# Kernel tuning notes

Measured on AMD Instinct MI355X. Metric: run time of the kernel, lower is better.

## Reference

```python
import jax, jax.numpy as jnp
import numpy as np

N_USERS = 150000
N_ENTITIES = 250000
CH = 64
N_REL = 17
N_FACTORS = 4
N_EDGES = 1_000_000
NNZ = 1_000_000
N_HOPS = 2


def setup_inputs() -> dict:
    key = jax.random.key(0)
    ks = jax.random.split(key, 10)
    user_emb = jax.random.normal(ks[0], (N_USERS, CH), jnp.float32) * 0.1
    entity_emb = jax.random.normal(ks[1], (N_ENTITIES, CH), jnp.float32) * 0.1
    latent_emb = jax.random.normal(ks[2], (N_FACTORS, CH), jnp.float32) * 0.1
    weight = jax.random.normal(ks[3], (N_REL - 1, CH), jnp.float32) * 0.1
    disen_weight_att = jax.random.normal(ks[4], (N_FACTORS, N_REL - 1), jnp.float32) * 0.1
    edge_index = jax.random.randint(ks[5], (2, N_EDGES), 0, N_ENTITIES)
    edge_type = jax.random.randint(ks[6], (N_EDGES,), 1, N_REL)  # in [1, N_REL-1]
    inter_row = jax.random.randint(ks[7], (NNZ,), 0, N_USERS)
    inter_col = jax.random.randint(ks[8], (NNZ,), 0, N_ENTITIES)
    inter_val = jax.random.uniform(ks[9], (NNZ,), jnp.float32)
    return {
        "user_emb": user_emb, "entity_emb": entity_emb, "latent_emb": latent_emb,
        "weight": weight, "disen_weight_att": disen_weight_att, "inter_val": inter_val,
        "edge_index": edge_index, "edge_type": edge_type,
        "inter_row": inter_row, "inter_col": inter_col,
    }


def _l2norm(x):
    # F.normalize(x, dim=1) with eps=1e-12
    n = jnp.linalg.norm(x, axis=1, keepdims=True)
    return x / jnp.maximum(n, 1e-12)


def reference(user_emb, entity_emb, latent_emb, weight, disen_weight_att,
              inter_val, edge_index, edge_type, inter_row, inter_col):
    n_entities = entity_emb.shape[0]
    n_users = user_emb.shape[0]
    head, tail = edge_index[0], edge_index[1]

    # _cul_cor with ind='cosine': sum_{i<j} cos(w_i, w_j)^2 over rows of disen_weight_att
    wn = disen_weight_att / jnp.linalg.norm(disen_weight_att, axis=1, keepdims=True)
    gram = (wn @ wn.T) ** 2  # [F, F]
    cor = jnp.sum(jnp.triu(gram, k=1))

    # constants across hops
    counts = jax.ops.segment_sum(jnp.ones(head.shape[0], jnp.float32), head,
                                 num_segments=n_entities)
    denom = jnp.maximum(counts, 1.0)[:, None]  # scatter_mean denominator (0 -> keep 0)
    disen_weight = jax.nn.softmax(disen_weight_att, axis=-1) @ weight  # [F, C]

    e, u = entity_emb, user_emb
    ent_res, usr_res = entity_emb, user_emb
    for _ in range(N_HOPS):
        # KG aggregate: per-edge gather, relation modulation, scatter_mean into heads
        neigh = e[tail] * weight[edge_type - 1]              # [E, C]
        entity_agg = jax.ops.segment_sum(neigh, head, num_segments=n_entities) / denom

        # user -> latent factor attention
        score = jax.nn.softmax(u @ latent_emb.T, axis=1)[:, :, None]  # [U, F, 1]

        # user aggregate: sparse interact_mat @ entity_emb
        user_agg = jax.ops.segment_sum(inter_val[:, None] * e[inter_col], inter_row,
                                       num_segments=n_users)  # [U, C]
        mix = jnp.sum(disen_weight[None, :, :] * score, axis=1)  # [U, C]
        user_agg = user_agg * mix + user_agg

        e = _l2norm(entity_agg)
        u = _l2norm(user_agg)
        ent_res = ent_res + e
        usr_res = usr_res + u
    return ent_res, usr_res, cor
```

## Files before the change

### kernel.cpp

```cpp
#include <hip/hip_runtime.h>
#include <hip/hip_bf16.h>

#define N_USERS    150000
#define N_ENTITIES 250000
#define CHN        64
#define N_RELM1    16
#define N_FACTORS  4
#define N_EDGES    1000000
#define NNZ_       1000000
#define NRECS      (N_EDGES + NNZ_)

#define BROWS      1024
#define RCAP       8192
#define RCAP_OUT   8192
#define EBUCKETS   245
#define USR0       (EBUCKETS * BROWS)
#define ROWS_EFF   (USR0 + N_USERS)
#define NB         392
#define TILE_A     4096
#define TA_THREADS 512
#define ITEMS_A    8

typedef float vf4 __attribute__((ext_vector_type(4)));

__device__ __forceinline__ unsigned short f2bf(float f) {
    unsigned u = __float_as_uint(f);
    return (unsigned short)((u + 0x7fffu + ((u >> 16) & 1u)) >> 16);
}

__global__ __launch_bounds__(512) void prep_small_kernel(const float* __restrict__ weight,
                                  const float* __restrict__ att,
                                  float* __restrict__ disenw,
                                  float* __restrict__ cor_out,
                                  int* __restrict__ bcur)
{
    int tid = threadIdx.x;
    if (tid < NB) bcur[tid] = tid * RCAP;

    if (tid < 256) {
        int f  = tid >> 6;
        int ch = tid & 63;
        float m = -1e30f;
        for (int r = 0; r < N_RELM1; ++r) m = fmaxf(m, att[f * N_RELM1 + r]);
        float ex[N_RELM1];
        float s = 0.f;
        for (int r = 0; r < N_RELM1; ++r) { ex[r] = expf(att[f * N_RELM1 + r] - m); s += ex[r]; }
        float inv = 1.f / s;
        float acc = 0.f;
        for (int r = 0; r < N_RELM1; ++r) acc += (ex[r] * inv) * weight[r * CHN + ch];
        disenw[f * CHN + ch] = acc;
    }

    if (tid == 0) {
        float wn[N_FACTORS][N_RELM1];
        for (int i = 0; i < N_FACTORS; ++i) {
            float ss = 0.f;
            for (int r = 0; r < N_RELM1; ++r) { float v = att[i * N_RELM1 + r]; ss += v * v; }
            float innv = 1.f / sqrtf(ss);
            for (int r = 0; r < N_RELM1; ++r) wn[i][r] = att[i * N_RELM1 + r] * innv;
        }
        float cor = 0.f;
        for (int i = 0; i < N_FACTORS; ++i)
            for (int j = i + 1; j < N_FACTORS; ++j) {
                float d = 0.f;
                for (int r = 0; r < N_RELM1; ++r) d += wn[i][r] * wn[j][r];
                cor += d * d;
            }
        cor_out[0] = cor;
    }
}

__global__ __launch_bounds__(256) void conv_bf16_kernel(const float4* __restrict__ src,
                                                        ushort4* __restrict__ dst, int n4)
{
    int i = blockIdx.x * 256 + threadIdx.x;
    if (i >= n4) return;
    float4 v = src[i];
    dst[i] = make_ushort4(f2bf(v.x), f2bf(v.y), f2bf(v.z), f2bf(v.w));
}

__global__ __launch_bounds__(TA_THREADS) void bin_pass_kernel(
    const int* __restrict__ head, const int* __restrict__ tail,
    const int* __restrict__ etype, const int* __restrict__ irow,
    const int* __restrict__ icol, const float* __restrict__ val,
    int* __restrict__ bcur, unsigned long long* __restrict__ binned)
{
    __shared__ int cntS[NB], startS[NB], gbase[NB];
    __shared__ unsigned long long buf[TILE_A];
    __shared__ unsigned short bk[TILE_A];

    int tid = threadIdx.x;
    if (tid < NB) cntS[tid] = 0;
    __syncthreads();

    int base = blockIdx.x * TILE_A;
    unsigned long long p[ITEMS_A];
    int bkt[ITEMS_A], rnk[ITEMS_A];
    #pragma unroll
    for (int j = 0; j < ITEMS_A; ++j) {
        int i = base + j * TA_THREADS + tid;
        bkt[j] = -1;
        if (i < NRECS) {
            int row; unsigned long long pay;
            if (i < N_EDGES) {
                row = head[i];
                pay = ((unsigned long long)(unsigned)(etype[i] - 1) << 18) | (unsigned)tail[i];
            } else {
                int jj = i - N_EDGES;
                row = USR0 + irow[jj];
                pay = ((unsigned long long)__float_as_uint(val[jj]) << 18) | (unsigned)icol[jj];
            }
            p[j] = pay | ((unsigned long long)(unsigned)(row & (BROWS - 1)) << 50);
            bkt[j] = row >> 10;
            rnk[j] = atomicAdd(&cntS[bkt[j]], 1);
        }
    }
    __syncthreads();
    if (tid == 0) {
        int s = 0;
        for (int b = 0; b < NB; ++b) { startS[b] = s; s += cntS[b]; }
    }
    __syncthreads();
    if (tid < NB && cntS[tid] > 0) gbase[tid] = atomicAdd(&bcur[tid], cntS[tid]);
    __syncthreads();

    #pragma unroll
    for (int j = 0; j < ITEMS_A; ++j) {
        if (bkt[j] >= 0) {
            int s = startS[bkt[j]] + rnk[j];
            buf[s] = p[j];
            bk[s] = (unsigned short)bkt[j];
        }
    }
    __syncthreads();

    int total = startS[NB - 1] + cntS[NB - 1];
    for (int s = tid; s < total; s += TA_THREADS) {
        int b = bk[s];
        int dst = gbase[b] + (s - startS[b]);
        if (dst < (b + 1) * RCAP) binned[dst] = buf[s];
    }
}

__global__ __launch_bounds__(512) void bucket_scatter_kernel(
    const unsigned long long* __restrict__ binned,
    const int* __restrict__ bcur,
    unsigned int* __restrict__ recsE,
    unsigned long long* __restrict__ recsU,
    unsigned int* __restrict__ cntoffs)
{
    __shared__ int rowcnt[BROWS];
    __shared__ int sA[512], sB[512];

    int tid = threadIdx.x;
    int b = blockIdx.x;
    rowcnt[2 * tid] = 0;
    rowcnt[2 * tid + 1] = 0;
    __syncthreads();

    int s0 = b * RCAP;
    int s1 = bcur[b];
    if (s1 > s0 + RCAP) s1 = s0 + RCAP;

    for (int i = s0 + tid; i < s1; i += 512) {
        int rowlo = (int)(binned[i] >> 50) & (BROWS - 1);
        atomicAdd(&rowcnt[rowlo], 1);
    }
    __syncthreads();

    int c0 = rowcnt[2 * tid];
    int c1 = rowcnt[2 * tid + 1];
    int pc0 = (c0 + 1) & ~1;
    int pc1 = (c1 + 1) & ~1;
    sA[tid] = pc0 + pc1;
    __syncthreads();
    int* src = sA; int* dst = sB;
    #pragma unroll
    for (int off = 1; off < 512; off <<= 1) {
        dst[tid] = src[tid] + ((tid >= off) ? src[tid - off] : 0);
        __syncthreads();
        int* tm = src; src = dst; dst = tm;
    }
    int excl = src[tid] - (pc0 + pc1);

    int gbaseOut = (b < EBUCKETS ? b : b - EBUCKETS) * RCAP_OUT;
    int grow = b * BROWS;
    cntoffs[grow + 2 * tid]     = ((unsigned)c0 << 22) | (unsigned)(gbaseOut + excl);
    cntoffs[grow + 2 * tid + 1] = ((unsigned)c1 << 22) | (unsigned)(gbaseOut + excl + pc0);
    __syncthreads();
    rowcnt[2 * tid] = excl;
    rowcnt[2 * tid + 1] = excl + pc0;
    __syncthreads();

    if (b < EBUCKETS) {
        for (int i = s0 + tid; i < s1; i += 512) {
            unsigned long long p = binned[i];
            int rowlo = (int)(p >> 50) & (BROWS - 1);
            int local = atomicAdd(&rowcnt[rowlo], 1);
            recsE[gbaseOut + local] = (unsigned)(p & ((1ull << 50) - 1));
        }
    } else {
        for (int i = s0 + tid; i < s1; i += 512) {
            unsigned long long p = binned[i];
            int rowlo = (int)(p >> 50) & (BROWS - 1);
            int local = atomicAdd(&rowcnt[rowlo], 1);
            recsU[gbaseOut + local] = p & ((1ull << 50) - 1);
        }
    }
}

__device__ __forceinline__ void fma8w(uint4 g, const float* __restrict__ w, float* acc) {
    acc[0] += __uint_as_float(g.x << 16)          * w[0];
    acc[1] += __uint_as_float(g.x & 0xffff0000u)  * w[1];
    acc[2] += __uint_as_float(g.y << 16)          * w[2];
    acc[3] += __uint_as_float(g.y & 0xffff0000u)  * w[3];
    acc[4] += __uint_as_float(g.z << 16)          * w[4];
    acc[5] += __uint_as_float(g.z & 0xffff0000u)  * w[5];
    acc[6] += __uint_as_float(g.w << 16)          * w[6];
    acc[7] += __uint_as_float(g.w & 0xffff0000u)  * w[7];
}
__device__ __forceinline__ void fma8v(uint4 g, float v, float* acc) {
    acc[0] += __uint_as_float(g.x << 16)          * v;
    acc[1] += __uint_as_float(g.x & 0xffff0000u)  * v;
    acc[2] += __uint_as_float(g.y << 16)          * v;
    acc[3] += __uint_as_float(g.y & 0xffff0000u)  * v;
    acc[4] += __uint_as_float(g.z << 16)          * v;
    acc[5] += __uint_as_float(g.z & 0xffff0000u)  * v;
    acc[6] += __uint_as_float(g.w << 16)          * v;
    acc[7] += __uint_as_float(g.w & 0xffff0000u)  * v;
}
__device__ __forceinline__ void bf8_unpack(uint4 g, float* o) {
    o[0] = __uint_as_float(g.x << 16); o[1] = __uint_as_float(g.x & 0xffff0000u);
    o[2] = __uint_as_float(g.y << 16); o[3] = __uint_as_float(g.y & 0xffff0000u);
    o[4] = __uint_as_float(g.z << 16); o[5] = __uint_as_float(g.z & 0xffff0000u);
    o[6] = __uint_as_float(g.w << 16); o[7] = __uint_as_float(g.w & 0xffff0000u);
}

template<int PASS>
__global__ __launch_bounds__(256) void hop_kernel(
    const unsigned short* __restrict__ ebf,
    const unsigned int* __restrict__ recsE,
    const unsigned long long* __restrict__ recsU,
    const unsigned int* __restrict__ cntoffs,
    const float* __restrict__ weight,
    const float* __restrict__ latent,
    const float* __restrict__ disenw,
    const float* __restrict__ u_emb,
    const float* __restrict__ e_emb,
    const unsigned short* __restrict__ ubfA,
    unsigned short* __restrict__ ebf_new,
    unsigned short* __restrict__ ubf_new,
    float* __restrict__ out_ent,
    float* __restrict__ out_usr)
{
    __shared__ float wl[N_RELM1 * CHN];
    for (int k = threadIdx.x; k < N_RELM1 * CHN; k += 256) wl[k] = weight[k];
    __syncthreads();

    unsigned idx = blockIdx.x * 256u + threadIdx.x;
    unsigned row = idx >> 3;
    int sub = idx & 7;
    int chb = sub * 8;

    float acc[8] = {0.f,0.f,0.f,0.f,0.f,0.f,0.f,0.f};

    if (row < N_ENTITIES) {
        unsigned co = cntoffs[row];
        int n = co >> 22;
        int start = co & 0x3FFFFF;
        int k = 0;
        for (; k + 4 <= n; k += 4) {
            uint2 ra = *(const uint2*)&recsE[start + k];
            uint2 rb = *(const uint2*)&recsE[start + k + 2];
            uint4 g0 = *(const uint4*)(ebf + (size_t)(ra.x & 0x3FFFF) * CHN + chb);
            uint4 g1 = *(const uint4*)(ebf + (size_t)(ra.y & 0x3FFFF) * CHN + chb);
            uint4 g2 = *(const uint4*)(ebf + (size_t)(rb.x & 0x3FFFF) * CHN + chb);
            uint4 g3 = *(const uint4*)(ebf + (size_t)(rb.y & 0x3FFFF) * CHN + chb);
            fma8w(g0, &wl[(ra.x >> 18) * CHN + chb], acc);
            fma8w(g1, &wl[(ra.y >> 18) * CHN + chb], acc);
            fma8w(g2, &wl[(rb.x >> 18) * CHN + chb], acc);
            fma8w(g3, &wl[(rb.y >> 18) * CHN + chb], acc);
        }
        for (; k < n; ++k) {
            unsigned r0 = recsE[start + k];
            uint4 g0 = *(const uint4*)(ebf + (size_t)(r0 & 0x3FFFF) * CHN + chb);
            fma8w(g0, &wl[(r0 >> 18) * CHN + chb], acc);
        }
        float inv_d = (n > 0) ? (1.f / (float)n) : 1.f;
        float ss = 0.f;
        #pragma unroll
        for (int i = 0; i < 8; ++i) { acc[i] *= inv_d; ss += acc[i] * acc[i]; }
        ss += __shfl_xor(ss, 1, 64);
        ss += __shfl_xor(ss, 2, 64);
        ss += __shfl_xor(ss, 4, 64);
        float innv = 1.f / fmaxf(sqrtf(ss), 1e-12f);
        float y[8];
        #pragma unroll
        for (int i = 0; i < 8; ++i) y[i] = acc[i] * innv;
        if (PASS == 1) {
            uint4 pk;
            pk.x = (unsigned)f2bf(y[0]) | ((unsigned)f2bf(y[1]) << 16);
            pk.y = (unsigned)f2bf(y[2]) | ((unsigned)f2bf(y[3]) << 16);
            pk.z = (unsigned)f2bf(y[4]) | ((unsigned)f2bf(y[5]) << 16);
            pk.w = (unsigned)f2bf(y[6]) | ((unsigned)f2bf(y[7]) << 16);
            *(uint4*)(ebf_new + (size_t)row * CHN + chb) = pk;
        } else {
            float y1[8];
            bf8_unpack(*(const uint4*)(ebf + (size_t)row * CHN + chb), y1);
            const vf4* bp = (const vf4*)&e_emb[(size_t)row * CHN + chb];
            vf4 b0 = __builtin_nontemporal_load(bp);
            vf4 b1 = __builtin_nontemporal_load(bp + 1);
            vf4* op = (vf4*)&out_ent[(size_t)row * CHN + chb];
            vf4 o0 = {b0.x + y1[0] + y[0], b0.y + y1[1] + y[1], b0.z + y1[2] + y[2], b0.w + y1[3] + y[3]};
            vf4 o1 = {b1.x + y1[4] + y[4], b1.y + y1[5] + y[5], b1.z + y1[6] + y[6], b1.w + y1[7] + y[7]};
            __builtin_nontemporal_store(o0, op);
            __builtin_nontemporal_store(o1, op + 1);
        }
    } else if (row >= USR0 && row < ROWS_EFF) {
        unsigned ur = row - USR0;
        unsigned co = cntoffs[row];
        int n = co >> 22;
        int start = co & 0x3FFFFF;

        float uo[8];
        if (PASS == 1) {
            const float4* up = (const float4*)&u_emb[(size_t)ur * CHN + chb];
            float4 a0 = up[0], a1 = up[1];
            uo[0]=a0.x; uo[1]=a0.y; uo[2]=a0.z; uo[3]=a0.w;
            uo[4]=a1.x; uo[5]=a1.y; uo[6]=a1.z; uo[7]=a1.w;
        } else {
            bf8_unpack(*(const uint4*)(ubfA + (size_t)ur * CHN + chb), uo);
        }

        float dotv[N_FACTORS];
        #pragma unroll
        for (int f = 0; f < N_FACTORS; ++f) {
            const float4* lp = (const float4*)&latent[f * CHN + chb];
            float4 l0 = lp[0], l1 = lp[1];
            float p = uo[0] * l0.x + uo[1] * l0.y + uo[2] * l0.z + uo[3] * l0.w
                    + uo[4] * l1.x + uo[5] * l1.y + uo[6] * l1.z + uo[7] * l1.w;
            p += __shfl_xor(p, 1, 64);
            p += __shfl_xor(p, 2, 64);
            p += __shfl_xor(p, 4, 64);
            dotv[f] = p;
        }
        float m = fmaxf(fmaxf(dotv[0], dotv[1]), fmaxf(dotv[2], dotv[3]));
        float es = 0.f;
        #pragma unroll
        for (int f = 0; f < N_FACTORS; ++f) { dotv[f] = expf(dotv[f] - m); es += dotv[f]; }
        float sinv = 1.f / es;
        float mix[8] = {0.f,0.f,0.f,0.f,0.f,0.f,0.f,0.f};
        #pragma unroll
        for (int f = 0; f < N_FACTORS; ++f) {
            float sc = dotv[f] * sinv;
            const float4* dp = (const float4*)&disenw[f * CHN + chb];
            float4 d0 = dp[0], d1 = dp[1];
            mix[0] += sc * d0.x; mix[1] += sc * d0.y; mix[2] += sc * d0.z; mix[3] += sc * d0.w;
            mix[4] += sc * d1.x; mix[5] += sc * d1.y; mix[6] += sc * d1.z; mix[7] += sc * d1.w;
        }

        int k = 0;
        for (; k + 4 <= n; k += 4) {
            ulonglong2 qa = *(const ulonglong2*)&recsU[start + k];
            ulonglong2 qb = *(const ulonglong2*)&recsU[start + k + 2];
            uint4 g0 = *(const uint4*)(ebf + (size_t)(qa.x & 0x3FFFFu) * CHN + chb);
            uint4 g1 = *(const uint4*)(ebf + (size_t)(qa.y & 0x3FFFFu) * CHN + chb);
            uint4 g2 = *(const uint4*)(ebf + (size_t)(qb.x & 0x3FFFFu) * CHN + chb);
            uint4 g3 = *(const uint4*)(ebf + (size_t)(qb.y & 0x3FFFFu) * CHN + chb);
            fma8v(g0, __uint_as_float((unsigned)(qa.x >> 18)), acc);
            fma8v(g1, __uint_as_float((unsigned)(qa.y >> 18)), acc);
            fma8v(g2, __uint_as_float((unsigned)(qb.x >> 18)), acc);
            fma8v(g3, __uint_as_float((unsigned)(qb.y >> 18)), acc);
        }
        for (; k < n; ++k) {
            unsigned long long q0 = recsU[start + k];
            uint4 g0 = *(const uint4*)(ebf + (size_t)(q0 & 0x3FFFFu) * CHN + chb);
            fma8v(g0, __uint_as_float((unsigned)(q0 >> 18)), acc);
        }
        float ss = 0.f;
        #pragma unroll
        for (int i = 0; i < 8; ++i) { acc[i] *= (1.f + mix[i]); ss += acc[i] * acc[i]; }
        ss += __shfl_xor(ss, 1, 64);
        ss += __shfl_xor(ss, 2, 64);
        ss += __shfl_xor(ss, 4, 64);
        float innv = 1.f / fmaxf(sqrtf(ss), 1e-12f);
        float y[8];
        #pragma unroll
        for (int i = 0; i < 8; ++i) y[i] = acc[i] * innv;
        if (PASS == 1) {
            uint4 pk;
            pk.x = (unsigned)f2bf(y[0]) | ((unsigned)f2bf(y[1]) << 16);
            pk.y = (unsigned)f2bf(y[2]) | ((unsigned)f2bf(y[3]) << 16);
            pk.z = (unsigned)f2bf(y[4]) | ((unsigned)f2bf(y[5]) << 16);
            pk.w = (unsigned)f2bf(y[6]) | ((unsigned)f2bf(y[7]) << 16);
            *(uint4*)(ubf_new + (size_t)ur * CHN + chb) = pk;
        } else {
            const vf4* bp = (const vf4*)&u_emb[(size_t)ur * CHN + chb];
            vf4 b0 = __builtin_nontemporal_load(bp);
            vf4 b1 = __builtin_nontemporal_load(bp + 1);
            vf4* op = (vf4*)&out_usr[(size_t)ur * CHN + chb];
            vf4 o0 = {b0.x + uo[0] + y[0], b0.y + uo[1] + y[1], b0.z + uo[2] + y[2], b0.w + uo[3] + y[3]};
            vf4 o1 = {b1.x + uo[4] + y[4], b1.y + uo[5] + y[5], b1.z + uo[6] + y[6], b1.w + uo[7] + y[7]};
            __builtin_nontemporal_store(o0, op);
            __builtin_nontemporal_store(o1, op + 1);
        }
    }
}

extern "C" void kernel_launch(void* const* d_in, const int* in_sizes, int n_in,
                              void* d_out, int out_size, void* d_ws, size_t ws_size,
                              hipStream_t stream) {
    const float* user_emb   = (const float*)d_in[0];
    const float* entity_emb = (const float*)d_in[1];
    const float* latent_emb = (const float*)d_in[2];
    const float* weight     = (const float*)d_in[3];
    const float* att        = (const float*)d_in[4];
    const float* inter_val  = (const float*)d_in[5];
    const int*   edge_index = (const int*)d_in[6];
    const int*   edge_type  = (const int*)d_in[7];
    const int*   inter_row  = (const int*)d_in[8];
    const int*   inter_col  = (const int*)d_in[9];

    const int* head = edge_index;
    const int* tail = edge_index + N_EDGES;

    float* out_ent = (float*)d_out;
    float* out_usr = out_ent + (size_t)N_ENTITIES * CHN;
    float* out_cor = out_usr + (size_t)N_USERS * CHN;

    char* ws = (char*)d_ws;
    unsigned short* ebf0   = (unsigned short*)ws;
    unsigned short* ebfA   = (unsigned short*)(ws + 32000000);
    unsigned short* ubfA   = (unsigned short*)(ws + 64000000);
    unsigned long long* binned = (unsigned long long*)(ws + 83200000);
    unsigned long long* recsU  = (unsigned long long*)(ws + 108890112);
    unsigned int* recsE    = (unsigned int*)(ws + 118523904);
    float* disenw          = (float*)(ws + 126552064);
    unsigned int* cntoffs  = (unsigned int*)(ws + 126553088);
    int*   bcur            = (int*)(ws + 128158720);

    prep_small_kernel<<<1, 512, 0, stream>>>(weight, att, disenw, out_cor, bcur);

    {
        int n4 = N_ENTITIES * CHN / 4;
        conv_bf16_kernel<<<(n4 + 255) / 256, 256, 0, stream>>>(
            (const float4*)entity_emb, (ushort4*)ebf0, n4);
    }

    const int binA_blocks = (NRECS + TILE_A - 1) / TILE_A;
    bin_pass_kernel<<<binA_blocks, TA_THREADS, 0, stream>>>(head, tail, edge_type,
                                                            inter_row, inter_col, inter_val,
                                                            bcur, binned);
    bucket_scatter_kernel<<<NB, 512, 0, stream>>>(binned, bcur, recsE, recsU, cntoffs);

    const int hop_blocks = (ROWS_EFF * 8 + 255) / 256;

    hop_kernel<1><<<hop_blocks, 256, 0, stream>>>(ebf0, recsE, recsU, cntoffs,
                                                  weight, latent_emb, disenw,
                                                  user_emb, entity_emb, nullptr,
                                                  ebfA, ubfA, nullptr, nullptr);

    hop_kernel<2><<<hop_blocks, 256, 0, stream>>>(ebfA, recsE, recsU, cntoffs,
                                                  weight, latent_emb, disenw,
                                                  user_emb, entity_emb, ubfA,
                                                  nullptr, nullptr, out_ent, out_usr);
}
```

Before: 227.1 us.

## Fuse setup kernels and inline first neighbor records into per-row headers

```diff
diff --git a/kernel.cpp b/kernel.cpp
--- a/kernel.cpp
+++ b/kernel.cpp
@@ -20,6 +20,9 @@
 #define TILE_A     4096
 #define TA_THREADS 512
 #define ITEMS_A    8
+#define BIN_BLOCKS 489
+#define CONV_N4    (N_ENTITIES * CHN / 4)
+#define CONV_BLOCKS ((CONV_N4 + 511) / 512)
 
 typedef float vf4 __attribute__((ext_vector_type(4)));
 
@@ -28,117 +31,111 @@
     return (unsigned short)((u + 0x7fffu + ((u >> 16) & 1u)) >> 16);
 }
 
-__global__ __launch_bounds__(512) void prep_small_kernel(const float* __restrict__ weight,
-                                  const float* __restrict__ att,
-                                  float* __restrict__ disenw,
-                                  float* __restrict__ cor_out,
-                                  int* __restrict__ bcur)
-{
-    int tid = threadIdx.x;
-    if (tid < NB) bcur[tid] = tid * RCAP;
-
-    if (tid < 256) {
-        int f  = tid >> 6;
-        int ch = tid & 63;
-        float m = -1e30f;
-        for (int r = 0; r < N_RELM1; ++r) m = fmaxf(m, att[f * N_RELM1 + r]);
-        float ex[N_RELM1];
-        float s = 0.f;
-        for (int r = 0; r < N_RELM1; ++r) { ex[r] = expf(att[f * N_RELM1 + r] - m); s += ex[r]; }
-        float inv = 1.f / s;
-        float acc = 0.f;
-        for (int r = 0; r < N_RELM1; ++r) acc += (ex[r] * inv) * weight[r * CHN + ch];
-        disenw[f * CHN + ch] = acc;
-    }
-
-    if (tid == 0) {
-        float wn[N_FACTORS][N_RELM1];
-        for (int i = 0; i < N_FACTORS; ++i) {
-            float ss = 0.f;
-            for (int r = 0; r < N_RELM1; ++r) { float v = att[i * N_RELM1 + r]; ss += v * v; }
-            float innv = 1.f / sqrtf(ss);
-            for (int r = 0; r < N_RELM1; ++r) wn[i][r] = att[i * N_RELM1 + r] * innv;
-        }
-        float cor = 0.f;
-        for (int i = 0; i < N_FACTORS; ++i)
-            for (int j = i + 1; j < N_FACTORS; ++j) {
-                float d = 0.f;
-                for (int r = 0; r < N_RELM1; ++r) d += wn[i][r] * wn[j][r];
-                cor += d * d;
-            }
-        cor_out[0] = cor;
-    }
-}
-
-__global__ __launch_bounds__(256) void conv_bf16_kernel(const float4* __restrict__ src,
-                                                        ushort4* __restrict__ dst, int n4)
-{
-    int i = blockIdx.x * 256 + threadIdx.x;
-    if (i >= n4) return;
-    float4 v = src[i];
-    dst[i] = make_ushort4(f2bf(v.x), f2bf(v.y), f2bf(v.z), f2bf(v.w));
-}
-
-__global__ __launch_bounds__(TA_THREADS) void bin_pass_kernel(
+__global__ __launch_bounds__(512) void build_kernel(
     const int* __restrict__ head, const int* __restrict__ tail,
     const int* __restrict__ etype, const int* __restrict__ irow,
     const int* __restrict__ icol, const float* __restrict__ val,
-    int* __restrict__ bcur, unsigned long long* __restrict__ binned)
+    int* __restrict__ bcur, unsigned long long* __restrict__ binned,
+    const float* __restrict__ weight, const float* __restrict__ att,
+    float* __restrict__ disenw, float* __restrict__ cor_out,
+    const float4* __restrict__ esrc, ushort4* __restrict__ ebf0)
 {
-    __shared__ int cntS[NB], startS[NB], gbase[NB];
-    __shared__ unsigned long long buf[TILE_A];
-    __shared__ unsigned short bk[TILE_A];
-
+    int blk = blockIdx.x;
     int tid = threadIdx.x;
-    if (tid < NB) cntS[tid] = 0;
-    __syncthreads();
-
-    int base = blockIdx.x * TILE_A;
-    unsigned long long p[ITEMS_A];
-    int bkt[ITEMS_A], rnk[ITEMS_A];
-    #pragma unroll
-    for (int j = 0; j < ITEMS_A; ++j) {
-        int i = base + j * TA_THREADS + tid;
-        bkt[j] = -1;
-        if (i < NRECS) {
-            int row; unsigned long long pay;
-            if (i < N_EDGES) {
-                row = head[i];
-                pay = ((unsigned long long)(unsigned)(etype[i] - 1) << 18) | (unsigned)tail[i];
-            } else {
-                int jj = i - N_EDGES;
-                row = USR0 + irow[jj];
-                pay = ((unsigned long long)__float_as_uint(val[jj]) << 18) | (unsigned)icol[jj];
+
+    if (blk < BIN_BLOCKS) {
+        __shared__ int cntS[NB], startS[NB], gbase[NB];
+        __shared__ unsigned long long buf[TILE_A];
+        __shared__ unsigned short bk[TILE_A];
+
+        if (tid < NB) cntS[tid] = 0;
+        __syncthreads();
+
+        int base = blk * TILE_A;
+        unsigned long long p[ITEMS_A];
+        int bkt[ITEMS_A], rnk[ITEMS_A];
+        #pragma unroll
+        for (int j = 0; j < ITEMS_A; ++j) {
+            int i = base + j * TA_THREADS + tid;
+            bkt[j] = -1;
+            if (i < NRECS) {
+                int row; unsigned long long pay;
+                if (i < N_EDGES) {
+                    row = head[i];
+                    pay = ((unsigned long long)(unsigned)(etype[i] - 1) << 18) | (unsigned)tail[i];
+                } else {
+                    int jj = i - N_EDGES;
+                    row = USR0 + irow[jj];
+                    pay = ((unsigned long long)__float_as_uint(val[jj]) << 18) | (unsigned)icol[jj];
+                }
+                p[j] = pay | ((unsigned long long)(unsigned)(row & (BROWS - 1)) << 50);
+                bkt[j] = row >> 10;
+                rnk[j] = atomicAdd(&cntS[bkt[j]], 1);
             }
-            p[j] = pay | ((unsigned long long)(unsigned)(row & (BROWS - 1)) << 50);
-            bkt[j] = row >> 10;
-            rnk[j] = atomicAdd(&cntS[bkt[j]], 1);
-        }
-    }
-    __syncthreads();
-    if (tid == 0) {
-        int s = 0;
-        for (int b = 0; b < NB; ++b) { startS[b] = s; s += cntS[b]; }
-    }
-    __syncthreads();
-    if (tid < NB && cntS[tid] > 0) gbase[tid] = atomicAdd(&bcur[tid], cntS[tid]);
-    __syncthreads();
-
-    #pragma unroll
-    for (int j = 0; j < ITEMS_A; ++j) {
-        if (bkt[j] >= 0) {
-            int s = startS[bkt[j]] + rnk[j];
-            buf[s] = p[j];
-            bk[s] = (unsigned short)bkt[j];
-        }
-    }
-    __syncthreads();
-
-    int total = startS[NB - 1] + cntS[NB - 1];
-    for (int s = tid; s < total; s += TA_THREADS) {
-        int b = bk[s];
-        int dst = gbase[b] + (s - startS[b]);
-        if (dst < (b + 1) * RCAP) binned[dst] = buf[s];
+        }
+        __syncthreads();
+        if (tid == 0) {
+            int s = 0;
+            for (int b = 0; b < NB; ++b) { startS[b] = s; s += cntS[b]; }
+        }
+        __syncthreads();
+        if (tid < NB && cntS[tid] > 0)
+            gbase[tid] = tid * RCAP + atomicAdd(&bcur[tid], cntS[tid]);
+        __syncthreads();
+
+        #pragma unroll
+        for (int j = 0; j < ITEMS_A; ++j) {
+            if (bkt[j] >= 0) {
+                int s = startS[bkt[j]] + rnk[j];
+                buf[s] = p[j];
+                bk[s] = (unsigned short)bkt[j];
+            }
+        }
+        __syncthreads();
+
+        int total = startS[NB - 1] + cntS[NB - 1];
+        for (int s = tid; s < total; s += TA_THREADS) {
+            int b = bk[s];
+            int dst = gbase[b] + (s - startS[b]);
+            if (dst < (b + 1) * RCAP) binned[dst] = buf[s];
+        }
+    } else if (blk == BIN_BLOCKS) {
+        if (tid < 256) {
+            int f  = tid >> 6;
+            int ch = tid & 63;
+            float m = -1e30f;
+            for (int r = 0; r < N_RELM1; ++r) m = fmaxf(m, att[f * N_RELM1 + r]);
+            float ex[N_RELM1];
+            float s = 0.f;
+            for (int r = 0; r < N_RELM1; ++r) { ex[r] = expf(att[f * N_RELM1 + r] - m); s += ex[r]; }
+            float inv = 1.f / s;
+            float acc = 0.f;
+            for (int r = 0; r < N_RELM1; ++r) acc += (ex[r] * inv) * weight[r * CHN + ch];
+            disenw[f * CHN + ch] = acc;
+        }
+        if (tid == 0) {
+            float wn[N_FACTORS][N_RELM1];
+            for (int i = 0; i < N_FACTORS; ++i) {
+                float ss = 0.f;
+                for (int r = 0; r < N_RELM1; ++r) { float v = att[i * N_RELM1 + r]; ss += v * v; }
+                float innv = 1.f / sqrtf(ss);
+                for (int r = 0; r < N_RELM1; ++r) wn[i][r] = att[i * N_RELM1 + r] * innv;
+            }
+            float cor = 0.f;
+            for (int i = 0; i < N_FACTORS; ++i)
+                for (int j = i + 1; j < N_FACTORS; ++j) {
+                    float d = 0.f;
+                    for (int r = 0; r < N_RELM1; ++r) d += wn[i][r] * wn[j][r];
+                    cor += d * d;
+                }
+            cor_out[0] = cor;
+        }
+    } else {
+        int i = (blk - BIN_BLOCKS - 1) * 512 + tid;
+        if (i < CONV_N4) {
+            float4 v = esrc[i];
+            ebf0[i] = make_ushort4(f2bf(v.x), f2bf(v.y), f2bf(v.z), f2bf(v.w));
+        }
     }
 }
 
@@ -147,20 +144,27 @@
     const int* __restrict__ bcur,
     unsigned int* __restrict__ recsE,
     unsigned long long* __restrict__ recsU,
-    unsigned int* __restrict__ cntoffs)
+    uint4* __restrict__ headerE,
+    uint4* __restrict__ headerU)
 {
     __shared__ int rowcnt[BROWS];
+    __shared__ int sExcl[BROWS];
     __shared__ int sA[512], sB[512];
+    __shared__ unsigned int hdr0[BROWS], hdr1[BROWS], hdr2[BROWS];
 
     int tid = threadIdx.x;
     int b = blockIdx.x;
     rowcnt[2 * tid] = 0;
     rowcnt[2 * tid + 1] = 0;
+    hdr0[2 * tid] = 0; hdr0[2 * tid + 1] = 0;
+    hdr1[2 * tid] = 0; hdr1[2 * tid + 1] = 0;
+    hdr2[2 * tid] = 0; hdr2[2 * tid + 1] = 0;
     __syncthreads();
 
     int s0 = b * RCAP;
-    int s1 = bcur[b];
-    if (s1 > s0 + RCAP) s1 = s0 + RCAP;
+    int nrec = bcur[b];
+    if (nrec > RCAP) nrec = RCAP;
+    int s1 = s0 + nrec;
 
     for (int i = s0 + tid; i < s1; i += 512) {
         int rowlo = (int)(binned[i] >> 50) & (BROWS - 1);
@@ -184,12 +188,11 @@
     int excl = src[tid] - (pc0 + pc1);
 
     int gbaseOut = (b < EBUCKETS ? b : b - EBUCKETS) * RCAP_OUT;
-    int grow = b * BROWS;
-    cntoffs[grow + 2 * tid]     = ((unsigned)c0 << 22) | (unsigned)(gbaseOut + excl);
-    cntoffs[grow + 2 * tid + 1] = ((unsigned)c1 << 22) | (unsigned)(gbaseOut + excl + pc0);
     __syncthreads();
     rowcnt[2 * tid] = excl;
     rowcnt[2 * tid + 1] = excl + pc0;
+    sExcl[2 * tid] = excl;
+    sExcl[2 * tid + 1] = excl + pc0;
     __syncthreads();
 
     if (b < EBUCKETS) {
@@ -197,14 +200,46 @@
             unsigned long long p = binned[i];
             int rowlo = (int)(p >> 50) & (BROWS - 1);
             int local = atomicAdd(&rowcnt[rowlo], 1);
-            recsE[gbaseOut + local] = (unsigned)(p & ((1ull << 50) - 1));
+            unsigned rec = (unsigned)(p & ((1ull << 50) - 1));
+            recsE[gbaseOut + local] = rec;
+            int rank = local - sExcl[rowlo];
+            if (rank == 0) hdr0[rowlo] = rec;
+            else if (rank == 1) hdr1[rowlo] = rec;
+            else if (rank == 2) hdr2[rowlo] = rec;
+        }
+        __syncthreads();
+        int grow = b * BROWS;
+        #pragma unroll
+        for (int t = 0; t < 2; ++t) {
+            int r = 2 * tid + t;
+            int row = grow + r;
+            if (row < N_ENTITIES) {
+                unsigned co = ((unsigned)((t == 0) ? c0 : c1) << 22) |
+                              (unsigned)(gbaseOut + sExcl[r]);
+                headerE[row] = make_uint4(co, hdr0[r], hdr1[r], hdr2[r]);
+            }
         }
     } else {
         for (int i = s0 + tid; i < s1; i += 512) {
             unsigned long long p = binned[i];
             int rowlo = (int)(p >> 50) & (BROWS - 1);
             int local = atomicAdd(&rowcnt[rowlo], 1);
-            recsU[gbaseOut + local] = p & ((1ull << 50) - 1);
+            unsigned long long rec = p & ((1ull << 50) - 1);
+            recsU[gbaseOut + local] = rec;
+            int rank = local - sExcl[rowlo];
+            if (rank == 0) { hdr0[rowlo] = (unsigned)rec; hdr1[rowlo] = (unsigned)(rec >> 32); }
+        }
+        __syncthreads();
+        int grow = b * BROWS - USR0;
+        #pragma unroll
+        for (int t = 0; t < 2; ++t) {
+            int r = 2 * tid + t;
+            int urow = grow + r;
+            if (urow >= 0 && urow < N_USERS) {
+                unsigned co = ((unsigned)((t == 0) ? c0 : c1) << 22) |
+                              (unsigned)(gbaseOut + sExcl[r]);
+                headerU[urow] = make_uint4(co, hdr0[r], hdr1[r], 0u);
+            }
         }
     }
 }
@@ -241,7 +276,8 @@
     const unsigned short* __restrict__ ebf,
     const unsigned int* __restrict__ recsE,
     const unsigned long long* __restrict__ recsU,
-    const unsigned int* __restrict__ cntoffs,
+    const uint4* __restrict__ headerE,
+    const uint4* __restrict__ headerU,
     const float* __restrict__ weight,
     const float* __restrict__ latent,
     const float* __restrict__ disenw,
@@ -265,21 +301,35 @@
     float acc[8] = {0.f,0.f,0.f,0.f,0.f,0.f,0.f,0.f};
 
     if (row < N_ENTITIES) {
-        unsigned co = cntoffs[row];
-        int n = co >> 22;
-        int start = co & 0x3FFFFF;
-        int k = 0;
+        uint4 h = headerE[row];
+        int n = h.x >> 22;
+        int start = h.x & 0x3FFFFF;
+        if (n > 0) {
+            uint4 g = *(const uint4*)(ebf + (size_t)(h.y & 0x3FFFF) * CHN + chb);
+            fma8w(g, &wl[(h.y >> 18) * CHN + chb], acc);
+        }
+        if (n > 1) {
+            uint4 g = *(const uint4*)(ebf + (size_t)(h.z & 0x3FFFF) * CHN + chb);
+            fma8w(g, &wl[(h.z >> 18) * CHN + chb], acc);
+        }
+        if (n > 2) {
+            uint4 g = *(const uint4*)(ebf + (size_t)(h.w & 0x3FFFF) * CHN + chb);
+            fma8w(g, &wl[(h.w >> 18) * CHN + chb], acc);
+        }
+        int k = 3;
         for (; k + 4 <= n; k += 4) {
-            uint2 ra = *(const uint2*)&recsE[start + k];
-            uint2 rb = *(const uint2*)&recsE[start + k + 2];
-            uint4 g0 = *(const uint4*)(ebf + (size_t)(ra.x & 0x3FFFF) * CHN + chb);
-            uint4 g1 = *(const uint4*)(ebf + (size_t)(ra.y & 0x3FFFF) * CHN + chb);
-            uint4 g2 = *(const uint4*)(ebf + (size_t)(rb.x & 0x3FFFF) * CHN + chb);
-            uint4 g3 = *(const uint4*)(ebf + (size_t)(rb.y & 0x3FFFF) * CHN + chb);
-            fma8w(g0, &wl[(ra.x >> 18) * CHN + chb], acc);
-            fma8w(g1, &wl[(ra.y >> 18) * CHN + chb], acc);
-            fma8w(g2, &wl[(rb.x >> 18) * CHN + chb], acc);
-            fma8w(g3, &wl[(rb.y >> 18) * CHN + chb], acc);
+            unsigned r0 = recsE[start + k];
+            unsigned r1 = recsE[start + k + 1];
+            unsigned r2 = recsE[start + k + 2];
+            unsigned r3 = recsE[start + k + 3];
+            uint4 g0 = *(const uint4*)(ebf + (size_t)(r0 & 0x3FFFF) * CHN + chb);
+            uint4 g1 = *(const uint4*)(ebf + (size_t)(r1 & 0x3FFFF) * CHN + chb);
+            uint4 g2 = *(const uint4*)(ebf + (size_t)(r2 & 0x3FFFF) * CHN + chb);
+            uint4 g3 = *(const uint4*)(ebf + (size_t)(r3 & 0x3FFFF) * CHN + chb);
+            fma8w(g0, &wl[(r0 >> 18) * CHN + chb], acc);
+            fma8w(g1, &wl[(r1 >> 18) * CHN + chb], acc);
+            fma8w(g2, &wl[(r2 >> 18) * CHN + chb], acc);
+            fma8w(g3, &wl[(r3 >> 18) * CHN + chb], acc);
         }
         for (; k < n; ++k) {
             unsigned r0 = recsE[start + k];
@@ -318,9 +368,35 @@
         }
     } else if (row >= USR0 && row < ROWS_EFF) {
         unsigned ur = row - USR0;
-        unsigned co = cntoffs[row];
-        int n = co >> 22;
-        int start = co & 0x3FFFFF;
+        uint4 h = headerU[ur];
+        int n = h.x >> 22;
+        int start = h.x & 0x3FFFFF;
+
+        if (n > 0) {
+            unsigned long long q = ((unsigned long long)h.z << 32) | h.y;
+            uint4 g = *(const uint4*)(ebf + (size_t)(q & 0x3FFFFu) * CHN + chb);
+            fma8v(g, __uint_as_float((unsigned)(q >> 18)), acc);
+        }
+        int k = 1;
+        for (; k + 4 <= n; k += 4) {
+            unsigned long long q0 = recsU[start + k];
+            unsigned long long q1 = recsU[start + k + 1];
+            unsigned long long q2 = recsU[start + k + 2];
+            unsigned long long q3 = recsU[start + k + 3];
+            uint4 g0 = *(const uint4*)(ebf + (size_t)(q0 & 0x3FFFFu) * CHN + chb);
+            uint4 g1 = *(const uint4*)(ebf + (size_t)(q1 & 0x3FFFFu) * CHN + chb);
+            uint4 g2 = *(const uint4*)(ebf + (size_t)(q2 & 0x3FFFFu) * CHN + chb);
+            uint4 g3 = *(const uint4*)(ebf + (size_t)(q3 & 0x3FFFFu) * CHN + chb);
+            fma8v(g0, __uint_as_float((unsigned)(q0 >> 18)), acc);
+            fma8v(g1, __uint_as_float((unsigned)(q1 >> 18)), acc);
+            fma8v(g2, __uint_as_float((unsigned)(q2 >> 18)), acc);
+            fma8v(g3, __uint_as_float((unsigned)(q3 >> 18)), acc);
+        }
+        for (; k < n; ++k) {
+            unsigned long long q0 = recsU[start + k];
+            uint4 g0 = *(const uint4*)(ebf + (size_t)(q0 & 0x3FFFFu) * CHN + chb);
+            fma8v(g0, __uint_as_float((unsigned)(q0 >> 18)), acc);
+        }
 
         float uo[8];
         if (PASS == 1) {
@@ -359,24 +435,6 @@
             mix[4] += sc * d1.x; mix[5] += sc * d1.y; mix[6] += sc * d1.z; mix[7] += sc * d1.w;
         }
 
-        int k = 0;
-        for (; k + 4 <= n; k += 4) {
-            ulonglong2 qa = *(const ulonglong2*)&recsU[start + k];
-            ulonglong2 qb = *(const ulonglong2*)&recsU[start + k + 2];
-            uint4 g0 = *(const uint4*)(ebf + (size_t)(qa.x & 0x3FFFFu) * CHN + chb);
-            uint4 g1 = *(const uint4*)(ebf + (size_t)(qa.y & 0x3FFFFu) * CHN + chb);
-            uint4 g2 = *(const uint4*)(ebf + (size_t)(qb.x & 0x3FFFFu) * CHN + chb);
-            uint4 g3 = *(const uint4*)(ebf + (size_t)(qb.y & 0x3FFFFu) * CHN + chb);
-            fma8v(g0, __uint_as_float((unsigned)(qa.x >> 18)), acc);
-            fma8v(g1, __uint_as_float((unsigned)(qa.y >> 18)), acc);
-            fma8v(g2, __uint_as_float((unsigned)(qb.x >> 18)), acc);
-            fma8v(g3, __uint_as_float((unsigned)(qb.y >> 18)), acc);
-        }
-        for (; k < n; ++k) {
-            unsigned long long q0 = recsU[start + k];
-            uint4 g0 = *(const uint4*)(ebf + (size_t)(q0 & 0x3FFFFu) * CHN + chb);
-            fma8v(g0, __uint_as_float((unsigned)(q0 >> 18)), acc);
-        }
         float ss = 0.f;
         #pragma unroll
         for (int i = 0; i < 8; ++i) { acc[i] *= (1.f + mix[i]); ss += acc[i] * acc[i]; }
@@ -436,31 +494,28 @@
     unsigned long long* recsU  = (unsigned long long*)(ws + 108890112);
     unsigned int* recsE    = (unsigned int*)(ws + 118523904);
     float* disenw          = (float*)(ws + 126552064);
-    unsigned int* cntoffs  = (unsigned int*)(ws + 126553088);
-    int*   bcur            = (int*)(ws + 128158720);
-
-    prep_small_kernel<<<1, 512, 0, stream>>>(weight, att, disenw, out_cor, bcur);
-
-    {
-        int n4 = N_ENTITIES * CHN / 4;
-        conv_bf16_kernel<<<(n4 + 255) / 256, 256, 0, stream>>>(
-            (const float4*)entity_emb, (ushort4*)ebf0, n4);
-    }
-
-    const int binA_blocks = (NRECS + TILE_A - 1) / TILE_A;
-    bin_pass_kernel<<<binA_blocks, TA_THREADS, 0, stream>>>(head, tail, edge_type,
-                                                            inter_row, inter_col, inter_val,
-                                                            bcur, binned);
-    bucket_scatter_kernel<<<NB, 512, 0, stream>>>(binned, bcur, recsE, recsU, cntoffs);
+    uint4* headerE         = (uint4*)(ws + 126553088);
+    uint4* headerU         = (uint4*)(ws + 130553088);
+    int*   bcur            = (int*)(ws + 132953088);
+
+    hipMemsetAsync(bcur, 0, NB * sizeof(int), stream);
+
+    build_kernel<<<BIN_BLOCKS + 1 + CONV_BLOCKS, 512, 0, stream>>>(
+        head, tail, edge_type, inter_row, inter_col, inter_val,
+        bcur, binned, weight, att, disenw, out_cor,
+        (const float4*)entity_emb, (ushort4*)ebf0);
+
+    bucket_scatter_kernel<<<NB, 512, 0, stream>>>(binned, bcur, recsE, recsU,
+                                                  headerE, headerU);
 
     const int hop_blocks = (ROWS_EFF * 8 + 255) / 256;
 
-    hop_kernel<1><<<hop_blocks, 256, 0, stream>>>(ebf0, recsE, recsU, cntoffs,
+    hop_kernel<1><<<hop_blocks, 256, 0, stream>>>(ebf0, recsE, recsU, headerE, headerU,
                                                   weight, latent_emb, disenw,
                                                   user_emb, entity_emb, nullptr,
                                                   ebfA, ubfA, nullptr, nullptr);
 
-    hop_kernel<2><<<hop_blocks, 256, 0, stream>>>(ebfA, recsE, recsU, cntoffs,
+    hop_kernel<2><<<hop_blocks, 256, 0, stream>>>(ebfA, recsE, recsU, headerE, headerU,
                                                   weight, latent_emb, disenw,
                                                   user_emb, entity_emb, ubfA,
                                                   nullptr, nullptr, out_ent, out_usr);
```

New measurement: 223.5 us. About the same (-1.6%).

## Fuse prep, bf16 conversion and binning into one build kernel

Applied to the files above, without the earlier changes.

```diff
diff --git a/kernel.cpp b/kernel.cpp
--- a/kernel.cpp
+++ b/kernel.cpp
@@ -20,6 +20,9 @@
 #define TILE_A     4096
 #define TA_THREADS 512
 #define ITEMS_A    8
+#define BIN_BLOCKS 489
+#define CONV_N4    (N_ENTITIES * CHN / 4)
+#define CONV_BLOCKS ((CONV_N4 + 511) / 512)
 
 typedef float vf4 __attribute__((ext_vector_type(4)));
 
@@ -28,117 +31,111 @@
     return (unsigned short)((u + 0x7fffu + ((u >> 16) & 1u)) >> 16);
 }
 
-__global__ __launch_bounds__(512) void prep_small_kernel(const float* __restrict__ weight,
-                                  const float* __restrict__ att,
-                                  float* __restrict__ disenw,
-                                  float* __restrict__ cor_out,
-                                  int* __restrict__ bcur)
-{
-    int tid = threadIdx.x;
-    if (tid < NB) bcur[tid] = tid * RCAP;
-
-    if (tid < 256) {
-        int f  = tid >> 6;
-        int ch = tid & 63;
-        float m = -1e30f;
-        for (int r = 0; r < N_RELM1; ++r) m = fmaxf(m, att[f * N_RELM1 + r]);
-        float ex[N_RELM1];
-        float s = 0.f;
-        for (int r = 0; r < N_RELM1; ++r) { ex[r] = expf(att[f * N_RELM1 + r] - m); s += ex[r]; }
-        float inv = 1.f / s;
-        float acc = 0.f;
-        for (int r = 0; r < N_RELM1; ++r) acc += (ex[r] * inv) * weight[r * CHN + ch];
-        disenw[f * CHN + ch] = acc;
-    }
-
-    if (tid == 0) {
-        float wn[N_FACTORS][N_RELM1];
-        for (int i = 0; i < N_FACTORS; ++i) {
-            float ss = 0.f;
-            for (int r = 0; r < N_RELM1; ++r) { float v = att[i * N_RELM1 + r]; ss += v * v; }
-            float innv = 1.f / sqrtf(ss);
-            for (int r = 0; r < N_RELM1; ++r) wn[i][r] = att[i * N_RELM1 + r] * innv;
-        }
-        float cor = 0.f;
-        for (int i = 0; i < N_FACTORS; ++i)
-            for (int j = i + 1; j < N_FACTORS; ++j) {
-                float d = 0.f;
-                for (int r = 0; r < N_RELM1; ++r) d += wn[i][r] * wn[j][r];
-                cor += d * d;
-            }
-        cor_out[0] = cor;
-    }
-}
-
-__global__ __launch_bounds__(256) void conv_bf16_kernel(const float4* __restrict__ src,
-                                                        ushort4* __restrict__ dst, int n4)
-{
-    int i = blockIdx.x * 256 + threadIdx.x;
-    if (i >= n4) return;
-    float4 v = src[i];
-    dst[i] = make_ushort4(f2bf(v.x), f2bf(v.y), f2bf(v.z), f2bf(v.w));
-}
-
-__global__ __launch_bounds__(TA_THREADS) void bin_pass_kernel(
+__global__ __launch_bounds__(512) void build_kernel(
     const int* __restrict__ head, const int* __restrict__ tail,
     const int* __restrict__ etype, const int* __restrict__ irow,
     const int* __restrict__ icol, const float* __restrict__ val,
-    int* __restrict__ bcur, unsigned long long* __restrict__ binned)
+    int* __restrict__ bcur, unsigned long long* __restrict__ binned,
+    const float* __restrict__ weight, const float* __restrict__ att,
+    float* __restrict__ disenw, float* __restrict__ cor_out,
+    const float4* __restrict__ esrc, ushort4* __restrict__ ebf0)
 {
-    __shared__ int cntS[NB], startS[NB], gbase[NB];
-    __shared__ unsigned long long buf[TILE_A];
-    __shared__ unsigned short bk[TILE_A];
-
+    int blk = blockIdx.x;
     int tid = threadIdx.x;
-    if (tid < NB) cntS[tid] = 0;
-    __syncthreads();
-
-    int base = blockIdx.x * TILE_A;
-    unsigned long long p[ITEMS_A];
-    int bkt[ITEMS_A], rnk[ITEMS_A];
-    #pragma unroll
-    for (int j = 0; j < ITEMS_A; ++j) {
-        int i = base + j * TA_THREADS + tid;
-        bkt[j] = -1;
-        if (i < NRECS) {
-            int row; unsigned long long pay;
-            if (i < N_EDGES) {
-                row = head[i];
-                pay = ((unsigned long long)(unsigned)(etype[i] - 1) << 18) | (unsigned)tail[i];
-            } else {
-                int jj = i - N_EDGES;
-                row = USR0 + irow[jj];
-                pay = ((unsigned long long)__float_as_uint(val[jj]) << 18) | (unsigned)icol[jj];
+
+    if (blk < BIN_BLOCKS) {
+        __shared__ int cntS[NB], startS[NB], gbase[NB];
+        __shared__ unsigned long long buf[TILE_A];
+        __shared__ unsigned short bk[TILE_A];
+
+        if (tid < NB) cntS[tid] = 0;
+        __syncthreads();
+
+        int base = blk * TILE_A;
+        unsigned long long p[ITEMS_A];
+        int bkt[ITEMS_A], rnk[ITEMS_A];
+        #pragma unroll
+        for (int j = 0; j < ITEMS_A; ++j) {
+            int i = base + j * TA_THREADS + tid;
+            bkt[j] = -1;
+            if (i < NRECS) {
+                int row; unsigned long long pay;
+                if (i < N_EDGES) {
+                    row = head[i];
+                    pay = ((unsigned long long)(unsigned)(etype[i] - 1) << 18) | (unsigned)tail[i];
+                } else {
+                    int jj = i - N_EDGES;
+                    row = USR0 + irow[jj];
+                    pay = ((unsigned long long)__float_as_uint(val[jj]) << 18) | (unsigned)icol[jj];
+                }
+                p[j] = pay | ((unsigned long long)(unsigned)(row & (BROWS - 1)) << 50);
+                bkt[j] = row >> 10;
+                rnk[j] = atomicAdd(&cntS[bkt[j]], 1);
             }
-            p[j] = pay | ((unsigned long long)(unsigned)(row & (BROWS - 1)) << 50);
-            bkt[j] = row >> 10;
-            rnk[j] = atomicAdd(&cntS[bkt[j]], 1);
-        }
-    }
-    __syncthreads();
-    if (tid == 0) {
-        int s = 0;
-        for (int b = 0; b < NB; ++b) { startS[b] = s; s += cntS[b]; }
-    }
-    __syncthreads();
-    if (tid < NB && cntS[tid] > 0) gbase[tid] = atomicAdd(&bcur[tid], cntS[tid]);
-    __syncthreads();
-
-    #pragma unroll
-    for (int j = 0; j < ITEMS_A; ++j) {
-        if (bkt[j] >= 0) {
-            int s = startS[bkt[j]] + rnk[j];
-            buf[s] = p[j];
-            bk[s] = (unsigned short)bkt[j];
-        }
-    }
-    __syncthreads();
-
-    int total = startS[NB - 1] + cntS[NB - 1];
-    for (int s = tid; s < total; s += TA_THREADS) {
-        int b = bk[s];
-        int dst = gbase[b] + (s - startS[b]);
-        if (dst < (b + 1) * RCAP) binned[dst] = buf[s];
+        }
+        __syncthreads();
+        if (tid == 0) {
+            int s = 0;
+            for (int b = 0; b < NB; ++b) { startS[b] = s; s += cntS[b]; }
+        }
+        __syncthreads();
+        if (tid < NB && cntS[tid] > 0)
+            gbase[tid] = tid * RCAP + atomicAdd(&bcur[tid], cntS[tid]);
+        __syncthreads();
+
+        #pragma unroll
+        for (int j = 0; j < ITEMS_A; ++j) {
+            if (bkt[j] >= 0) {
+                int s = startS[bkt[j]] + rnk[j];
+                buf[s] = p[j];
+                bk[s] = (unsigned short)bkt[j];
+            }
+        }
+        __syncthreads();
+
+        int total = startS[NB - 1] + cntS[NB - 1];
+        for (int s = tid; s < total; s += TA_THREADS) {
+            int b = bk[s];
+            int dst = gbase[b] + (s - startS[b]);
+            if (dst < (b + 1) * RCAP) binned[dst] = buf[s];
+        }
+    } else if (blk == BIN_BLOCKS) {
+        if (tid < 256) {
+            int f  = tid >> 6;
+            int ch = tid & 63;
+            float m = -1e30f;
+            for (int r = 0; r < N_RELM1; ++r) m = fmaxf(m, att[f * N_RELM1 + r]);
+            float ex[N_RELM1];
+            float s = 0.f;
+            for (int r = 0; r < N_RELM1; ++r) { ex[r] = expf(att[f * N_RELM1 + r] - m); s += ex[r]; }
+            float inv = 1.f / s;
+            float acc = 0.f;
+            for (int r = 0; r < N_RELM1; ++r) acc += (ex[r] * inv) * weight[r * CHN + ch];
+            disenw[f * CHN + ch] = acc;
+        }
+        if (tid == 0) {
+            float wn[N_FACTORS][N_RELM1];
+            for (int i = 0; i < N_FACTORS; ++i) {
+                float ss = 0.f;
+                for (int r = 0; r < N_RELM1; ++r) { float v = att[i * N_RELM1 + r]; ss += v * v; }
+                float innv = 1.f / sqrtf(ss);
+                for (int r = 0; r < N_RELM1; ++r) wn[i][r] = att[i * N_RELM1 + r] * innv;
+            }
+            float cor = 0.f;
+            for (int i = 0; i < N_FACTORS; ++i)
+                for (int j = i + 1; j < N_FACTORS; ++j) {
+                    float d = 0.f;
+                    for (int r = 0; r < N_RELM1; ++r) d += wn[i][r] * wn[j][r];
+                    cor += d * d;
+                }
+            cor_out[0] = cor;
+        }
+    } else {
+        int i = (blk - BIN_BLOCKS - 1) * 512 + tid;
+        if (i < CONV_N4) {
+            float4 v = esrc[i];
+            ebf0[i] = make_ushort4(f2bf(v.x), f2bf(v.y), f2bf(v.z), f2bf(v.w));
+        }
     }
 }
 
@@ -159,8 +156,9 @@
     __syncthreads();
 
     int s0 = b * RCAP;
-    int s1 = bcur[b];
-    if (s1 > s0 + RCAP) s1 = s0 + RCAP;
+    int nrec = bcur[b];
+    if (nrec > RCAP) nrec = RCAP;
+    int s1 = s0 + nrec;
 
     for (int i = s0 + tid; i < s1; i += 512) {
         int rowlo = (int)(binned[i] >> 50) & (BROWS - 1);
@@ -246,7 +244,7 @@
     const float* __restrict__ latent,
     const float* __restrict__ disenw,
     const float* __restrict__ u_emb,
-    const float* __restrict__ e_emb,
+    const unsigned short* __restrict__ ebase,
     const unsigned short* __restrict__ ubfA,
     unsigned short* __restrict__ ebf_new,
     unsigned short* __restrict__ ubf_new,
@@ -307,12 +305,11 @@
         } else {
             float y1[8];
             bf8_unpack(*(const uint4*)(ebf + (size_t)row * CHN + chb), y1);
-            const vf4* bp = (const vf4*)&e_emb[(size_t)row * CHN + chb];
-            vf4 b0 = __builtin_nontemporal_load(bp);
-            vf4 b1 = __builtin_nontemporal_load(bp + 1);
+            float b[8];
+            bf8_unpack(*(const uint4*)(ebase + (size_t)row * CHN + chb), b);
             vf4* op = (vf4*)&out_ent[(size_t)row * CHN + chb];
-            vf4 o0 = {b0.x + y1[0] + y[0], b0.y + y1[1] + y[1], b0.z + y1[2] + y[2], b0.w + y1[3] + y[3]};
-            vf4 o1 = {b1.x + y1[4] + y[4], b1.y + y1[5] + y[5], b1.z + y1[6] + y[6], b1.w + y1[7] + y[7]};
+            vf4 o0 = {b[0] + y1[0] + y[0], b[1] + y1[1] + y[1], b[2] + y1[2] + y[2], b[3] + y1[3] + y[3]};
+            vf4 o1 = {b[4] + y1[4] + y[4], b[5] + y1[5] + y[5], b[6] + y1[6] + y[6], b[7] + y1[7] + y[7]};
             __builtin_nontemporal_store(o0, op);
             __builtin_nontemporal_store(o1, op + 1);
         }
@@ -439,29 +436,24 @@
     unsigned int* cntoffs  = (unsigned int*)(ws + 126553088);
     int*   bcur            = (int*)(ws + 128158720);
 
-    prep_small_kernel<<<1, 512, 0, stream>>>(weight, att, disenw, out_cor, bcur);
-
-    {
-        int n4 = N_ENTITIES * CHN / 4;
-        conv_bf16_kernel<<<(n4 + 255) / 256, 256, 0, stream>>>(
-            (const float4*)entity_emb, (ushort4*)ebf0, n4);
-    }
-
-    const int binA_blocks = (NRECS + TILE_A - 1) / TILE_A;
-    bin_pass_kernel<<<binA_blocks, TA_THREADS, 0, stream>>>(head, tail, edge_type,
-                                                            inter_row, inter_col, inter_val,
-                                                            bcur, binned);
+    hipMemsetAsync(bcur, 0, NB * sizeof(int), stream);
+
+    build_kernel<<<BIN_BLOCKS + 1 + CONV_BLOCKS, 512, 0, stream>>>(
+        head, tail, edge_type, inter_row, inter_col, inter_val,
+        bcur, binned, weight, att, disenw, out_cor,
+        (const float4*)entity_emb, (ushort4*)ebf0);
+
     bucket_scatter_kernel<<<NB, 512, 0, stream>>>(binned, bcur, recsE, recsU, cntoffs);
 
     const int hop_blocks = (ROWS_EFF * 8 + 255) / 256;
 
     hop_kernel<1><<<hop_blocks, 256, 0, stream>>>(ebf0, recsE, recsU, cntoffs,
                                                   weight, latent_emb, disenw,
-                                                  user_emb, entity_emb, nullptr,
+                                                  user_emb, nullptr, nullptr,
                                                   ebfA, ubfA, nullptr, nullptr);
 
     hop_kernel<2><<<hop_blocks, 256, 0, stream>>>(ebfA, recsE, recsU, cntoffs,
                                                   weight, latent_emb, disenw,
-                                                  user_emb, entity_emb, ubfA,
+                                                  user_emb, ebf0, ubfA,
                                                   nullptr, nullptr, out_ent, out_usr);
 }
```

After: 213.9 us. 1.06x faster.
